# Performance work log

Hardware: AMD Instinct MI355X
Metric: run time of the kernel (lower is better)

Reference implementation:

```python
import jax, jax.numpy as jnp
import numpy as np

N, F, H, E, R = 100000, 256, 64, 800000, 7
EPS = 1e-5

def _layernorm(x, g, b):
    mu = jnp.mean(x, axis=-1, keepdims=True)
    var = jnp.mean((x - mu) ** 2, axis=-1, keepdims=True)
    return (x - mu) * jax.lax.rsqrt(var + EPS) * g + b

def setup_inputs() -> dict:
    key = jax.random.key(0)
    ks = jax.random.split(key, 16)
    block_features = jax.random.normal(ks[0], (N, F), dtype=jnp.float32)
    src = jax.random.randint(ks[1], (E,), 0, N).astype(jnp.float32)
    dst = jax.random.randint(ks[2], (E,), 0, N).astype(jnp.float32)
    rel = jax.random.randint(ks[3], (E,), 0, R).astype(jnp.float32)
    w = jax.random.uniform(ks[4], (E,), dtype=jnp.float32)
    typed_edges = jnp.stack([src, dst, rel, w], axis=1)  # [E,4]
    def lin(k, fan_in, fan_out):
        s = 1.0 / np.sqrt(fan_in)
        k1, k2 = jax.random.split(k)
        return (jax.random.uniform(k1, (fan_in, fan_out), jnp.float32, -s, s),
                jax.random.uniform(k2, (fan_out,), jnp.float32, -s, s))
    W1, b1 = lin(ks[5], F, H)
    W2, b2 = lin(ks[6], H, H)
    rel_emb = jax.random.normal(ks[7], (R, H), dtype=jnp.float32)
    Wm1, bm1 = lin(ks[8], 3 * H + 1, H)
    Wm2, bm2 = lin(ks[9], H, H)
    Wg1, bg1 = lin(ks[10], 2 * H, H)
    Wg2, bg2 = lin(ks[11], H, H)
    return dict(block_features=block_features, typed_edges=typed_edges,
                W1=W1, b1=b1, g1=jnp.ones(H), be1=jnp.zeros(H), W2=W2, b2=b2,
                rel_emb=rel_emb, Wm1=Wm1, bm1=bm1, Wm2=Wm2, bm2=bm2,
                gn=jnp.ones(H), bn=jnp.zeros(H), Wg1=Wg1, bg1=bg1, Wg2=Wg2, bg2=bg2)

def reference(block_features, typed_edges, W1, b1, g1, be1, W2, b2, rel_emb,
              Wm1, bm1, Wm2, bm2, gn, bn, Wg1, bg1, Wg2, bg2):
    # node_proj: Linear -> LN -> ReLU -> Linear -> ReLU
    h = jax.nn.relu(_layernorm(block_features @ W1 + b1, g1, be1))
    h = jax.nn.relu(h @ W2 + b2)  # [N,H]
    src = typed_edges[:, 0].astype(jnp.int32)
    dst = typed_edges[:, 1].astype(jnp.int32)
    rel = typed_edges[:, 2].astype(jnp.int32)
    w = typed_edges[:, 3:4]  # [E,1]
    m_in = jnp.concatenate([h[src], h[dst], rel_emb[rel], w], axis=-1)  # [E,3H+1]
    msg = jax.nn.relu(m_in @ Wm1 + bm1) @ Wm2 + bm2  # [E,H]
    agg = jax.ops.segment_sum(msg, dst, num_segments=h.shape[0])  # [N,H]
    nodes = _layernorm(h + agg, gn, bn)
    g = jnp.concatenate([nodes.mean(axis=0), nodes.max(axis=0)], axis=-1)  # [2H]
    return jax.nn.relu(g @ Wg1 + bg1) @ Wg2 + bg2  # [H]
```

## Files before the change

### kernel.cpp

```cpp
#include <hip/hip_runtime.h>

typedef unsigned short u16;
typedef unsigned int   u32;
typedef __attribute__((ext_vector_type(8))) short bf16x8;
typedef __attribute__((ext_vector_type(4))) float f32x4;

#define EPS 1e-5f
#define MFMA(a,b,c) __builtin_amdgcn_mfma_f32_16x16x32_bf16(a,b,c,0,0,0)

constexpr int OB_b1=0, OB_g1=64, OB_be1=128, OB_b2=192, OB_bm1=256, OB_w192=320,
              OB_bm2=384, OB_gn=448, OB_bn=512, OB_bg1=576, OB_bg2=640,
              OB_Wg1=704, OB_Wg2=8896, WB_TOT=12992;
constexpr int FR_Wm1=0;
constexpr int FR_Wm2=12288;
constexpr int FR_rel=16384;
constexpr int FR_W1 =16960;
constexpr int FR_W2 =33344;
constexpr int FR_TOT=37440;

__device__ __forceinline__ float bf2f(u32 u) { return __uint_as_float(u << 16); }
__device__ __forceinline__ u16 f2bf(float f) {
  u32 b = __float_as_uint(f);
  return (u16)((b + 0x7fffu + ((b >> 16) & 1u)) >> 16);
}
__device__ __forceinline__ u32 fkey(float f) {
  u32 b = __float_as_uint(f);
  return (b & 0x80000000u) ? ~b : (b | 0x80000000u);
}

__device__ __forceinline__ void gld_lds16(const void* g, void* l) {
  __builtin_amdgcn_global_load_lds(
      (const __attribute__((address_space(1))) void*)g,
      (__attribute__((address_space(3))) void*)l, 16, 0, 0);
}

__launch_bounds__(256)
__global__ void k_prep(const float* __restrict__ W1, const float* __restrict__ b1,
                       const float* __restrict__ g1, const float* __restrict__ be1,
                       const float* __restrict__ W2, const float* __restrict__ b2,
                       const float* __restrict__ rel_emb,
                       const float* __restrict__ Wm1, const float* __restrict__ bm1,
                       const float* __restrict__ Wm2, const float* __restrict__ bm2,
                       const float* __restrict__ gn, const float* __restrict__ bn,
                       const float* __restrict__ Wg1, const float* __restrict__ bg1,
                       const float* __restrict__ Wg2, const float* __restrict__ bg2,
                       float* __restrict__ wbuf, u16* __restrict__ frags,
                       const float* __restrict__ te, int* __restrict__ cnt,
                       float* __restrict__ gsum, u32* __restrict__ gmax, int E, int N) {
  int tid = blockIdx.x * 256 + threadIdx.x;
  int nth = gridDim.x * 256;
  for (int i = tid; i < 64; i += nth) {
    wbuf[OB_b1 + i] = b1[i];   wbuf[OB_g1 + i] = g1[i];
    wbuf[OB_be1 + i] = be1[i]; wbuf[OB_b2 + i] = b2[i];
    wbuf[OB_bm1 + i] = bm1[i]; wbuf[OB_w192 + i] = Wm1[192 * 64 + i];
    wbuf[OB_bm2 + i] = bm2[i]; wbuf[OB_gn + i] = gn[i];
    wbuf[OB_bn + i] = bn[i];   wbuf[OB_bg1 + i] = bg1[i];
    wbuf[OB_bg2 + i] = bg2[i];
    gsum[i] = 0.f; gmax[i] = 0u;
  }
  for (int i = tid; i < 8192; i += nth) wbuf[OB_Wg1 + i] = Wg1[i];
  for (int i = tid; i < 4096; i += nth) wbuf[OB_Wg2 + i] = Wg2[i];
  for (int idx = tid; idx < 16384; idx += nth) {
    int f = idx >> 9, L = (idx >> 3) & 63, j = idx & 7;
    int k = (f >> 2) * 32 + ((L >> 4) << 3) + j, n = ((f & 3) << 4) + (L & 15);
    frags[FR_W1 + idx] = f2bf(W1[k * 64 + n]);
  }
  for (int idx = tid; idx < 4096; idx += nth) {
    int f = idx >> 9, L = (idx >> 3) & 63, j = idx & 7;
    int k = (f >> 2) * 32 + ((L >> 4) << 3) + j, n = ((f & 3) << 4) + (L & 15);
    frags[FR_W2 + idx] = f2bf(W2[k * 64 + n]);
  }
  for (int idx = tid; idx < 12288; idx += nth) {
    int f = idx >> 9, L = (idx >> 3) & 63, j = idx & 7;
    int k = (f >> 2) * 32 + ((L >> 4) << 3) + j, n = ((f & 3) << 4) + (L & 15);
    frags[FR_Wm1 + idx] = f2bf(Wm1[k * 64 + n]);
  }
  for (int idx = tid; idx < 4096; idx += nth) {
    int f = idx >> 9, L = (idx >> 3) & 63, j = idx & 7;
    int k = (f >> 2) * 32 + ((L >> 4) << 3) + j, n = ((f & 3) << 4) + (L & 15);
    frags[FR_Wm2 + idx] = f2bf(Wm2[k * 64 + n]);
  }
  for (int idx = tid; idx < 576; idx += nth) {
    int r = idx / 80, c = idx % 80;
    frags[FR_rel + idx] = (r < 7 && c < 64) ? f2bf(rel_emb[r * 64 + c]) : (u16)0;
  }
  for (int e = tid; e < E; e += nth) {
    float4 v = *(const float4*)(te + (size_t)e * 4);
    int d = min(max((int)v.y, 0), N - 1);
    atomicAdd(&cnt[d], 1);
  }
}

#define SCH 512
__launch_bounds__(256)
__global__ void k_scan1(const int* __restrict__ cnt, int* __restrict__ bsum, int N) {
  __shared__ int sd[256];
  int b = blockIdx.x, t = threadIdx.x, base = b * SCH;
  int i0 = base + 2 * t, i1 = i0 + 1;
  int a = 0;
  if (i0 < N) a += cnt[i0];
  if (i1 < N) a += cnt[i1];
  sd[t] = a; __syncthreads();
  for (int s = 128; s > 0; s >>= 1) { if (t < s) sd[t] += sd[t + s]; __syncthreads(); }
  if (t == 0) bsum[b] = sd[0];
}

__launch_bounds__(256)
__global__ void k_scan2(const int* __restrict__ bsum, int* __restrict__ bofs,
                        int* __restrict__ ofs, int NBLK, int N) {
  __shared__ int sd[256];
  int t = threadIdx.x;
  int K = (NBLK + 255) / 256;
  int loc = 0;
  for (int k = 0; k < K; k++) { int i = t * K + k; if (i < NBLK) loc += bsum[i]; }
  sd[t] = loc; __syncthreads();
  for (int s = 1; s < 256; s <<= 1) {
    int o = 0; if (t >= s) o = sd[t - s];
    __syncthreads(); sd[t] += o; __syncthreads();
  }
  int excl = sd[t] - loc;
  int run = excl;
  for (int k = 0; k < K; k++) {
    int i = t * K + k;
    if (i < NBLK) { bofs[i] = run; run += bsum[i]; }
  }
  if (t == 255) ofs[N] = sd[255];
}

__launch_bounds__(256)
__global__ void k_scan3(const int* __restrict__ bofs, int* __restrict__ ofs,
                        int* __restrict__ cur, int N) {
  __shared__ int sd[256];
  int b = blockIdx.x, t = threadIdx.x, base = b * SCH;
  int i0 = base + 2 * t, i1 = i0 + 1;
  int a0 = (i0 < N) ? cur[i0] : 0, a1 = (i1 < N) ? cur[i1] : 0;
  int pair = a0 + a1;
  sd[t] = pair; __syncthreads();
  for (int s = 1; s < 256; s <<= 1) {
    int o = 0; if (t >= s) o = sd[t - s];
    __syncthreads(); sd[t] += o; __syncthreads();
  }
  int excl = sd[t] - pair + bofs[b];
  if (i0 < N) { ofs[i0] = excl;      cur[i0] = excl; }
  if (i1 < N) { ofs[i1] = excl + a0; cur[i1] = excl + a0; }
}

__launch_bounds__(256)
__global__ void k_place(const float* __restrict__ te, int* __restrict__ cur,
                        uint4* __restrict__ sorted, int E, int N) {
  int i = blockIdx.x * 256 + threadIdx.x, st = gridDim.x * 256;
  for (int e = i; e < E; e += st) {
    float4 v = *(const float4*)(te + (size_t)e * 4);
    int s = min(max((int)v.x, 0), N - 1);
    int d = min(max((int)v.y, 0), N - 1);
    int r = min(max((int)v.z, 0), 6);
    int pos = atomicAdd(&cur[d], 1);
    uint4 rec; rec.x = (u32)s; rec.y = (u32)d; rec.z = (u32)r; rec.w = __float_as_uint(v.w);
    sorted[pos] = rec;
  }
}

__launch_bounds__(256, 4)
__global__ void k_h(const float* __restrict__ X, const float* __restrict__ wbuf,
                    const u16* __restrict__ frags, u16* __restrict__ hb,
                    float* __restrict__ agg, int N) {
  __shared__ __align__(16) float xb[2][16 * 256];
  __shared__ __align__(16) u16 st[16 * 72];
  __shared__ float sred[2][16][4];

  int lane = threadIdx.x & 63, wave = threadIdx.x >> 6;
  int m = lane & 15, quad = lane >> 4;
  int col = wave * 16 + m;

  bf16x8 bw1[8], bw2[2];
  #pragma unroll
  for (int ks = 0; ks < 8; ks++)
    bw1[ks] = *(const bf16x8*)(frags + FR_W1 + ((ks * 4 + wave) * 64 + lane) * 8);
  #pragma unroll
  for (int ks = 0; ks < 2; ks++)
    bw2[ks] = *(const bf16x8*)(frags + FR_W2 + ((ks * 4 + wave) * 64 + lane) * 8);

  float b1v = wbuf[OB_b1 + col], g1v = wbuf[OB_g1 + col];
  float be1v = wbuf[OB_be1 + col], b2v = wbuf[OB_b2 + col];

  int ntiles = (N + 15) / 16;
  int xorm = (m & 7) << 4;

  auto stage = [&](int t, int buf) {
    int n0s = t * 16;
    #pragma unroll
    for (int i = 0; i < 4; i++) {
      int r = wave * 4 + i;
      int nr = min(n0s + r, N - 1);
      const char* src = (const char*)(X + (size_t)nr * 256);
      int soff = (lane * 16) ^ ((r & 7) << 4);
      gld_lds16(src + soff, (char*)&xb[buf][0] + r * 1024);
    }
  };

  int cur = 0;
  if (blockIdx.x < ntiles) stage(blockIdx.x, 0);

  for (int t = blockIdx.x; t < ntiles; t += gridDim.x) {
    __syncthreads();
    if (t + (int)gridDim.x < ntiles) stage(t + gridDim.x, cur ^ 1);

    int n0 = t * 16;
    const char* xp = (const char*)&xb[cur][0];

    f32x4 acc = {};
    #pragma unroll
    for (int ks = 0; ks < 8; ks++) {
      int base = m * 1024 + ks * 128 + quad * 32;
      float4 u0 = *(const float4*)(xp + (base ^ xorm));
      float4 u1 = *(const float4*)(xp + ((base + 16) ^ xorm));
      bf16x8 a;
      a[0] = (short)f2bf(u0.x); a[1] = (short)f2bf(u0.y);
      a[2] = (short)f2bf(u0.z); a[3] = (short)f2bf(u0.w);
      a[4] = (short)f2bf(u1.x); a[5] = (short)f2bf(u1.y);
      a[6] = (short)f2bf(u1.z); a[7] = (short)f2bf(u1.w);
      acc = MFMA(a, bw1[ks], acc);
    }

    float vv[4];
    #pragma unroll
    for (int r = 0; r < 4; r++) vv[r] = acc[r] + b1v;
    #pragma unroll
    for (int r = 0; r < 4; r++) {
      float s = vv[r], q = vv[r] * vv[r];
      #pragma unroll
      for (int mk = 8; mk >= 1; mk >>= 1) {
        s += __shfl_xor(s, mk, 64);
        q += __shfl_xor(q, mk, 64);
      }
      if (m == 0) { sred[0][quad * 4 + r][wave] = s; sred[1][quad * 4 + r][wave] = q; }
    }
    __syncthreads();
    #pragma unroll
    for (int r = 0; r < 4; r++) {
      int row = quad * 4 + r;
      float4 S = *(const float4*)&sred[0][row][0];
      float4 Q = *(const float4*)&sred[1][row][0];
      float mu = (S.x + S.y + S.z + S.w) * (1.f / 64.f);
      float vq = (Q.x + Q.y + Q.z + Q.w) * (1.f / 64.f) - mu * mu;
      float rs = rsqrtf(fmaxf(vq, 0.f) + EPS);
      float h1 = fmaxf(fmaf((vv[r] - mu) * rs, g1v, be1v), 0.f);
      st[row * 72 + col] = f2bf(h1);
    }
    __syncthreads();

    f32x4 acc2 = {};
    #pragma unroll
    for (int ks = 0; ks < 2; ks++) {
      bf16x8 a2 = *(const bf16x8*)(st + m * 72 + ks * 32 + quad * 8);
      acc2 = MFMA(a2, bw2[ks], acc2);
    }
    #pragma unroll
    for (int r = 0; r < 4; r++) {
      int row = n0 + quad * 4 + r;
      if (row < N) {
        float hv = fmaxf(acc2[r] + b2v, 0.f);
        hb[(size_t)row * 64 + col] = f2bf(hv);
        agg[(size_t)row * 64 + col] = hv;
      }
    }
    cur ^= 1;
  }
}

__launch_bounds__(512, 4)
__global__ void k_edge(const uint4* __restrict__ sorted, const u16* __restrict__ hb,
                       const float* __restrict__ wbuf, const u16* __restrict__ frags,
                       float* __restrict__ agg, int E, int N) {
  __shared__ __align__(16) u16 sWm1[24 * 512];
  __shared__ __align__(16) u16 sWm2[8 * 512];
  __shared__ __align__(16) u16 srel[576];
  __shared__ __align__(16) float st32[8][16 * 68];
  __shared__ int sdst[8][16];

  {
    const uint4* s1 = (const uint4*)(frags + FR_Wm1);
    uint4* d1 = (uint4*)sWm1;
    for (int i = threadIdx.x; i < 1536; i += 512) d1[i] = s1[i];
    const uint4* s2 = (const uint4*)(frags + FR_Wm2);
    uint4* d2 = (uint4*)sWm2;
    for (int i = threadIdx.x; i < 512; i += 512) d2[i] = s2[i];
    const uint4* s3 = (const uint4*)(frags + FR_rel);
    uint4* d3 = (uint4*)srel;
    for (int i = threadIdx.x; i < 72; i += 512) d3[i] = s3[i];
  }
  __syncthreads();

  int lane = threadIdx.x & 63, wave = threadIdx.x >> 6;
  int m = lane & 15, quad = lane >> 4, koff = quad * 8, col0 = m;
  float* st = st32[wave];
  int* dstS = sdst[wave];

  float bm1v[4], w192v[4], bm2v[4];
  #pragma unroll
  for (int nt = 0; nt < 4; nt++) {
    int c = nt * 16 + col0;
    bm1v[nt] = wbuf[OB_bm1 + c];
    w192v[nt] = wbuf[OB_w192 + c];
    bm2v[nt] = wbuf[OB_bm2 + c];
  }

  int ntiles = (E + 15) >> 4;
  int gw = blockIdx.x * 8 + wave, nw = gridDim.x * 8;
  int per = (ntiles + nw - 1) / nw;
  int tile = gw * per, tend = min(tile + per, ntiles);

  int cd = -1; float cv = 0.f;

  for (; tile < tend; tile++) {
    int e0 = tile * 16;
    int src = 0, dstv = 0, rel = 0; float w = 0.f;
    if (lane < 16) {
      int e = e0 + lane;
      uint4 rc = sorted[min(e, E - 1)];
      src = (int)rc.x; dstv = (int)rc.y; rel = (int)rc.z; w = __uint_as_float(rc.w);
      dstS[lane] = (e < E) ? dstv : -1;
    }
    int sm = __shfl(src, m, 64), dm = __shfl(dstv, m, 64), rm = __shfl(rel, m, 64);

    const u16* hs = hb + (size_t)sm * 64;
    const u16* hd = hb + (size_t)dm * 64;
    bf16x8 af[6];
    af[0] = *(const bf16x8*)(hs + koff);
    af[1] = *(const bf16x8*)(hs + 32 + koff);
    af[2] = *(const bf16x8*)(hd + koff);
    af[3] = *(const bf16x8*)(hd + 32 + koff);
    af[4] = *(const bf16x8*)(srel + rm * 80 + koff);
    af[5] = *(const bf16x8*)(srel + rm * 80 + 32 + koff);

    f32x4 acc[4] = {};
    #pragma unroll
    for (int ks = 0; ks < 6; ks++)
      #pragma unroll
      for (int nt = 0; nt < 4; nt++) {
        bf16x8 b = *(const bf16x8*)(sWm1 + (ks * 4 + nt) * 512 + lane * 8);
        acc[nt] = MFMA(af[ks], b, acc[nt]);
      }

    float wrow[4];
    #pragma unroll
    for (int r = 0; r < 4; r++) wrow[r] = __shfl(w, quad * 4 + r, 64);
    #pragma unroll
    for (int nt = 0; nt < 4; nt++)
      #pragma unroll
      for (int r = 0; r < 4; r++) {
        float v = fmaf(wrow[r], w192v[nt], acc[nt][r] + bm1v[nt]);
        st[(quad * 4 + r) * 68 + nt * 16 + col0] = fmaxf(v, 0.f);
      }
    __builtin_amdgcn_wave_barrier();

    f32x4 acc2[4] = {};
    #pragma unroll
    for (int ks = 0; ks < 2; ks++) {
      float4 p0 = *(const float4*)(st + m * 68 + ks * 32 + koff);
      float4 p1 = *(const float4*)(st + m * 68 + ks * 32 + koff + 4);
      bf16x8 a2;
      a2[0] = (short)f2bf(p0.x); a2[1] = (short)f2bf(p0.y);
      a2[2] = (short)f2bf(p0.z); a2[3] = (short)f2bf(p0.w);
      a2[4] = (short)f2bf(p1.x); a2[5] = (short)f2bf(p1.y);
      a2[6] = (short)f2bf(p1.z); a2[7] = (short)f2bf(p1.w);
      #pragma unroll
      for (int nt = 0; nt < 4; nt++) {
        bf16x8 b = *(const bf16x8*)(sWm2 + (ks * 4 + nt) * 512 + lane * 8);
        acc2[nt] = MFMA(a2, b, acc2[nt]);
      }
    }
    __builtin_amdgcn_wave_barrier();

    #pragma unroll
    for (int nt = 0; nt < 4; nt++)
      #pragma unroll
      for (int r = 0; r < 4; r++)
        st[(quad * 4 + r) * 68 + nt * 16 + col0] = acc2[nt][r] + bm2v[nt];
    __builtin_amdgcn_wave_barrier();

    #pragma unroll
    for (int r = 0; r < 16; r++) {
      int d = dstS[r];
      float v = st[r * 68 + lane];
      if (d != cd) {
        if (cd >= 0) atomicAdd(agg + (size_t)cd * 64 + lane, cv);
        cd = d; cv = 0.f;
      }
      if (d >= 0) cv += v;
    }
    __builtin_amdgcn_wave_barrier();
  }
  if (cd >= 0) atomicAdd(agg + (size_t)cd * 64 + lane, cv);
}

__launch_bounds__(256)
__global__ void k_nodes(const float* __restrict__ agg, const float* __restrict__ wbuf,
                        float* __restrict__ gsum, u32* __restrict__ gmax, int N) {
  int lane = threadIdx.x & 63, wave = threadIdx.x >> 6;
  int r4 = lane >> 4, c4 = (lane & 15) * 4;
  float4 gnv = *(const float4*)(wbuf + OB_gn + c4);
  float4 bnv = *(const float4*)(wbuf + OB_bn + c4);
  int wid = blockIdx.x * 4 + wave, nw = gridDim.x * 4;
  float sj[4] = {0.f, 0.f, 0.f, 0.f};
  float mj[4] = {-3.0e38f, -3.0e38f, -3.0e38f, -3.0e38f};
  for (int base = wid * 4; base < N; base += nw * 4) {
    int row = base + r4;
    bool ok = row < N;
    float4 av = ok ? *(const float4*)(agg + (size_t)row * 64 + c4)
                   : make_float4(0.f, 0.f, 0.f, 0.f);
    float s = av.x + av.y + av.z + av.w;
    #pragma unroll
    for (int mk = 8; mk >= 1; mk >>= 1) s += __shfl_xor(s, mk, 64);
    float mu = s * (1.f / 64.f);
    float d0 = av.x - mu, d1 = av.y - mu, d2 = av.z - mu, d3 = av.w - mu;
    float q = d0 * d0 + d1 * d1 + d2 * d2 + d3 * d3;
    #pragma unroll
    for (int mk = 8; mk >= 1; mk >>= 1) q += __shfl_xor(q, mk, 64);
    float rs = rsqrtf(q * (1.f / 64.f) + EPS);
    if (ok) {
      float t0 = fmaf(d0 * rs, gnv.x, bnv.x);
      float t1 = fmaf(d1 * rs, gnv.y, bnv.y);
      float t2 = fmaf(d2 * rs, gnv.z, bnv.z);
      float t3 = fmaf(d3 * rs, gnv.w, bnv.w);
      sj[0] += t0; mj[0] = fmaxf(mj[0], t0);
      sj[1] += t1; mj[1] = fmaxf(mj[1], t1);
      sj[2] += t2; mj[2] = fmaxf(mj[2], t2);
      sj[3] += t3; mj[3] = fmaxf(mj[3], t3);
    }
  }
  #pragma unroll
  for (int j = 0; j < 4; j++) {
    sj[j] += __shfl_xor(sj[j], 16, 64);
    sj[j] += __shfl_xor(sj[j], 32, 64);
    mj[j] = fmaxf(mj[j], __shfl_xor(mj[j], 16, 64));
    mj[j] = fmaxf(mj[j], __shfl_xor(mj[j], 32, 64));
  }
  __shared__ float bs[4][64], bm[4][64];
  if (lane < 16) {
    #pragma unroll
    for (int j = 0; j < 4; j++) { bs[wave][c4 + j] = sj[j]; bm[wave][c4 + j] = mj[j]; }
  }
  __syncthreads();
  if (threadIdx.x < 64) {
    int c = threadIdx.x;
    float ts = bs[0][c] + bs[1][c] + bs[2][c] + bs[3][c];
    float tm = fmaxf(fmaxf(bm[0][c], bm[1][c]), fmaxf(bm[2][c], bm[3][c]));
    atomicAdd(gsum + c, ts);
    atomicMax(gmax + c, fkey(tm));
  }
}

__launch_bounds__(128)
__global__ void k_final(const float* __restrict__ wbuf, const float* __restrict__ gsum,
                        const u32* __restrict__ gmax, float* __restrict__ out, int N) {
  __shared__ float g[128];
  __shared__ float y1[64];
  int t = threadIdx.x;
  if (t < 64) {
    g[t] = gsum[t] / (float)N;
  } else {
    u32 k = gmax[t - 64];
    u32 b = (k & 0x80000000u) ? (k & 0x7fffffffu) : ~k;
    g[t] = __uint_as_float(b);
  }
  __syncthreads();
  if (t < 64) {
    float a = wbuf[OB_bg1 + t];
    for (int i = 0; i < 128; i++) a = fmaf(g[i], wbuf[OB_Wg1 + i * 64 + t], a);
    y1[t] = fmaxf(a, 0.f);
  }
  __syncthreads();
  if (t < 64) {
    float a = wbuf[OB_bg2 + t];
    for (int k = 0; k < 64; k++) a = fmaf(y1[k], wbuf[OB_Wg2 + k * 64 + t], a);
    out[t] = a;
  }
}

extern "C" void kernel_launch(void* const* d_in, const int* in_sizes, int n_in,
                              void* d_out, int out_size, void* d_ws, size_t ws_size,
                              hipStream_t stream) {
  const int N = in_sizes[0] / 256;
  const int E = in_sizes[1] / 4;
  const int NBLK = (N + SCH - 1) / SCH;

  char* ws = (char*)d_ws;
  size_t p = 0;
  auto rup = [](size_t x) { return (x + 255) & ~(size_t)255; };
  uint4* sorted = (uint4*)(ws + p); p += rup((size_t)E * 16);
  float* agg    = (float*)(ws + p); p += rup((size_t)N * 64 * 4);
  u16*   hb     = (u16*)(ws + p);   p += rup((size_t)N * 128);
  int*   ofs    = (int*)(ws + p);   p += rup((size_t)(N + 1) * 4);
  int*   cur    = (int*)(ws + p);   p += rup((size_t)N * 4);
  int*   bsum   = (int*)(ws + p);   p += rup((size_t)(NBLK + 1) * 4);
  int*   bofs   = (int*)(ws + p);   p += rup((size_t)(NBLK + 1) * 4);
  float* gsum   = (float*)(ws + p); p += 256;
  u32*   gmax   = (u32*)(ws + p);   p += 256;
  float* wbuf   = (float*)(ws + p); p += rup((size_t)WB_TOT * 4);
  u16*   frags  = (u16*)(ws + p);   p += rup((size_t)FR_TOT * 2);

  const float* X  = (const float*)d_in[0];
  const float* te = (const float*)d_in[1];

  hipMemsetAsync(cur, 0, (size_t)N * 4, stream);
  hipLaunchKernelGGL(k_prep, dim3(1024), dim3(256), 0, stream,
                     (const float*)d_in[2], (const float*)d_in[3], (const float*)d_in[4],
                     (const float*)d_in[5], (const float*)d_in[6], (const float*)d_in[7],
                     (const float*)d_in[8], (const float*)d_in[9], (const float*)d_in[10],
                     (const float*)d_in[11], (const float*)d_in[12], (const float*)d_in[13],
                     (const float*)d_in[14], (const float*)d_in[15], (const float*)d_in[16],
                     (const float*)d_in[17], (const float*)d_in[18], wbuf, frags,
                     te, cur, gsum, gmax, E, N);

  hipLaunchKernelGGL(k_scan1, dim3(NBLK), dim3(256), 0, stream, cur, bsum, N);
  hipLaunchKernelGGL(k_scan2, dim3(1), dim3(256), 0, stream, bsum, bofs, ofs, NBLK, N);
  hipLaunchKernelGGL(k_scan3, dim3(NBLK), dim3(256), 0, stream, bofs, ofs, cur, N);
  hipLaunchKernelGGL(k_place, dim3(1024), dim3(256), 0, stream, te, cur, sorted, E, N);

  hipLaunchKernelGGL(k_h, dim3(1024), dim3(256), 0, stream, X, wbuf, frags, hb, agg, N);
  hipLaunchKernelGGL(k_edge, dim3(512), dim3(512), 0, stream, sorted, hb, wbuf, frags, agg, E, N);
  hipLaunchKernelGGL(k_nodes, dim3(2048), dim3(256), 0, stream, agg, wbuf, gsum, gmax, N);
  hipLaunchKernelGGL(k_final, dim3(1), dim3(128), 0, stream, wbuf, gsum, gmax, (float*)d_out, N);
}
```

Baseline: 400.6 us.

## Merge scan kernels, prefetch edge tiles, fuse final MLP into nodes kernel

Replaces the three-pass prefix scan with one single-block 1024-thread scan and folds the final MLP into k_nodes using a last-block ticket, removing several kernel launches. k_edge now prefetches the next tile's edge records and gathered features while the current tile's MFMAs run. It keeps the hidden activations as bf16 in LDS instead of fp32, and moves the scatter through register shuffles instead of an LDS round trip. Occupancy and grid size for k_edge go up (launch bounds 5, grid 768). The single-block scan serializes about 100 elements per thread, and the prefetch adds register pressure.

New measurement: 594.2 us. +48.3%, slower.

```diff
diff --git a/kernel.cpp b/kernel.cpp
--- a/kernel.cpp
+++ b/kernel.cpp
@@ -46,9 +46,11 @@
                        const float* __restrict__ Wg2, const float* __restrict__ bg2,
                        float* __restrict__ wbuf, u16* __restrict__ frags,
                        const float* __restrict__ te, int* __restrict__ cnt,
-                       float* __restrict__ gsum, u32* __restrict__ gmax, int E, int N) {
+                       float* __restrict__ gsum, u32* __restrict__ gmax,
+                       int* __restrict__ ticket, int E, int N) {
   int tid = blockIdx.x * 256 + threadIdx.x;
   int nth = gridDim.x * 256;
+  if (tid == 0) *ticket = 0;
   for (int i = tid; i < 64; i += nth) {
     wbuf[OB_b1 + i] = b1[i];   wbuf[OB_g1 + i] = g1[i];
     wbuf[OB_be1 + i] = be1[i]; wbuf[OB_b2 + i] = b2[i];
@@ -91,58 +93,27 @@
   }
 }
 
-#define SCH 512
-__launch_bounds__(256)
-__global__ void k_scan1(const int* __restrict__ cnt, int* __restrict__ bsum, int N) {
-  __shared__ int sd[256];
-  int b = blockIdx.x, t = threadIdx.x, base = b * SCH;
-  int i0 = base + 2 * t, i1 = i0 + 1;
-  int a = 0;
-  if (i0 < N) a += cnt[i0];
-  if (i1 < N) a += cnt[i1];
-  sd[t] = a; __syncthreads();
-  for (int s = 128; s > 0; s >>= 1) { if (t < s) sd[t] += sd[t + s]; __syncthreads(); }
-  if (t == 0) bsum[b] = sd[0];
-}
-
-__launch_bounds__(256)
-__global__ void k_scan2(const int* __restrict__ bsum, int* __restrict__ bofs,
-                        int* __restrict__ ofs, int NBLK, int N) {
-  __shared__ int sd[256];
+__launch_bounds__(1024)
+__global__ void k_scan(int* __restrict__ cur, int N) {
+  __shared__ int sd[1024];
   int t = threadIdx.x;
-  int K = (NBLK + 255) / 256;
+  int K = (N + 1023) / 1024;
+  int beg = t * K, end = min(beg + K, N);
   int loc = 0;
-  for (int k = 0; k < K; k++) { int i = t * K + k; if (i < NBLK) loc += bsum[i]; }
+  for (int i = beg; i < end; i++) loc += cur[i];
   sd[t] = loc; __syncthreads();
-  for (int s = 1; s < 256; s <<= 1) {
-    int o = 0; if (t >= s) o = sd[t - s];
-    __syncthreads(); sd[t] += o; __syncthreads();
-  }
-  int excl = sd[t] - loc;
-  int run = excl;
-  for (int k = 0; k < K; k++) {
-    int i = t * K + k;
-    if (i < NBLK) { bofs[i] = run; run += bsum[i]; }
-  }
-  if (t == 255) ofs[N] = sd[255];
-}
-
-__launch_bounds__(256)
-__global__ void k_scan3(const int* __restrict__ bofs, int* __restrict__ ofs,
-                        int* __restrict__ cur, int N) {
-  __shared__ int sd[256];
-  int b = blockIdx.x, t = threadIdx.x, base = b * SCH;
-  int i0 = base + 2 * t, i1 = i0 + 1;
-  int a0 = (i0 < N) ? cur[i0] : 0, a1 = (i1 < N) ? cur[i1] : 0;
-  int pair = a0 + a1;
-  sd[t] = pair; __syncthreads();
-  for (int s = 1; s < 256; s <<= 1) {
-    int o = 0; if (t >= s) o = sd[t - s];
-    __syncthreads(); sd[t] += o; __syncthreads();
-  }
-  int excl = sd[t] - pair + bofs[b];
-  if (i0 < N) { ofs[i0] = excl;      cur[i0] = excl; }
-  if (i1 < N) { ofs[i1] = excl + a0; cur[i1] = excl + a0; }
+  for (int s = 1; s < 1024; s <<= 1) {
+    int o = (t >= s) ? sd[t - s] : 0;
+    __syncthreads();
+    sd[t] += o;
+    __syncthreads();
+  }
+  int run = sd[t] - loc;
+  for (int i = beg; i < end; i++) {
+    int c = cur[i];
+    cur[i] = run;
+    run += c;
+  }
 }
 
 __launch_bounds__(256)
@@ -268,15 +239,14 @@
   }
 }
 
-__launch_bounds__(512, 4)
+__launch_bounds__(512, 5)
 __global__ void k_edge(const uint4* __restrict__ sorted, const u16* __restrict__ hb,
                        const float* __restrict__ wbuf, const u16* __restrict__ frags,
                        float* __restrict__ agg, int E, int N) {
   __shared__ __align__(16) u16 sWm1[24 * 512];
   __shared__ __align__(16) u16 sWm2[8 * 512];
   __shared__ __align__(16) u16 srel[576];
-  __shared__ __align__(16) float st32[8][16 * 68];
-  __shared__ int sdst[8][16];
+  __shared__ __align__(16) u16 stt[8][16 * 72];
 
   {
     const uint4* s1 = (const uint4*)(frags + FR_Wm1);
@@ -293,8 +263,8 @@
 
   int lane = threadIdx.x & 63, wave = threadIdx.x >> 6;
   int m = lane & 15, quad = lane >> 4, koff = quad * 8, col0 = m;
-  float* st = st32[wave];
-  int* dstS = sdst[wave];
+  int nthi = lane >> 4;
+  u16* stw = stt[wave];
 
   float bm1v[4], w192v[4], bm2v[4];
   #pragma unroll
@@ -306,32 +276,44 @@
   }
 
   int ntiles = (E + 15) >> 4;
-  int gw = blockIdx.x * 8 + wave, nw = gridDim.x * 8;
-  int per = (ntiles + nw - 1) / nw;
+  int gw = blockIdx.x * 8 + wave, nwv = gridDim.x * 8;
+  int per = (ntiles + nwv - 1) / nwv;
   int tile = gw * per, tend = min(tile + per, ntiles);
 
   int cd = -1; float cv = 0.f;
-
-  for (; tile < tend; tile++) {
-    int e0 = tile * 16;
-    int src = 0, dstv = 0, rel = 0; float w = 0.f;
+  int dstv = -1; float wv = 0.f;
+  bf16x8 af[6];
+
+  if (tile < tend) {
+    int srcv = 0, relv = 0;
     if (lane < 16) {
-      int e = e0 + lane;
+      int e = tile * 16 + lane;
       uint4 rc = sorted[min(e, E - 1)];
-      src = (int)rc.x; dstv = (int)rc.y; rel = (int)rc.z; w = __uint_as_float(rc.w);
-      dstS[lane] = (e < E) ? dstv : -1;
-    }
-    int sm = __shfl(src, m, 64), dm = __shfl(dstv, m, 64), rm = __shfl(rel, m, 64);
-
+      srcv = (int)rc.x; dstv = (e < E) ? (int)rc.y : -1;
+      relv = (int)rc.z; wv = __uint_as_float(rc.w);
+    }
+    int sm = __shfl(srcv, m, 64), dmv = __shfl(dstv, m, 64), rm = __shfl(relv, m, 64);
+    int dmg = dmv < 0 ? 0 : dmv;
     const u16* hs = hb + (size_t)sm * 64;
-    const u16* hd = hb + (size_t)dm * 64;
-    bf16x8 af[6];
+    const u16* hd = hb + (size_t)dmg * 64;
     af[0] = *(const bf16x8*)(hs + koff);
     af[1] = *(const bf16x8*)(hs + 32 + koff);
     af[2] = *(const bf16x8*)(hd + koff);
     af[3] = *(const bf16x8*)(hd + 32 + koff);
     af[4] = *(const bf16x8*)(srel + rm * 80 + koff);
     af[5] = *(const bf16x8*)(srel + rm * 80 + 32 + koff);
+  }
+
+  for (; tile < tend; tile++) {
+    bool hasnext = (tile + 1) < tend;
+
+    int srcn = 0, dstn = -1, reln = 0; float wn = 0.f;
+    if (hasnext && lane < 16) {
+      int e = (tile + 1) * 16 + lane;
+      uint4 rc = sorted[min(e, E - 1)];
+      srcn = (int)rc.x; dstn = (e < E) ? (int)rc.y : -1;
+      reln = (int)rc.z; wn = __uint_as_float(rc.w);
+    }
 
     f32x4 acc[4] = {};
     #pragma unroll
@@ -342,28 +324,35 @@
         acc[nt] = MFMA(af[ks], b, acc[nt]);
       }
 
+    if (hasnext) {
+      int sm = __shfl(srcn, m, 64), dmv = __shfl(dstn, m, 64), rm = __shfl(reln, m, 64);
+      int dmg = dmv < 0 ? 0 : dmv;
+      const u16* hs = hb + (size_t)sm * 64;
+      const u16* hd = hb + (size_t)dmg * 64;
+      af[0] = *(const bf16x8*)(hs + koff);
+      af[1] = *(const bf16x8*)(hs + 32 + koff);
+      af[2] = *(const bf16x8*)(hd + koff);
+      af[3] = *(const bf16x8*)(hd + 32 + koff);
+      af[4] = *(const bf16x8*)(srel + rm * 80 + koff);
+      af[5] = *(const bf16x8*)(srel + rm * 80 + 32 + koff);
+    }
+
     float wrow[4];
     #pragma unroll
-    for (int r = 0; r < 4; r++) wrow[r] = __shfl(w, quad * 4 + r, 64);
+    for (int r = 0; r < 4; r++) wrow[r] = __shfl(wv, quad * 4 + r, 64);
     #pragma unroll
     for (int nt = 0; nt < 4; nt++)
       #pragma unroll
       for (int r = 0; r < 4; r++) {
         float v = fmaf(wrow[r], w192v[nt], acc[nt][r] + bm1v[nt]);
-        st[(quad * 4 + r) * 68 + nt * 16 + col0] = fmaxf(v, 0.f);
+        stw[(quad * 4 + r) * 72 + nt * 16 + col0] = f2bf(fmaxf(v, 0.f));
       }
     __builtin_amdgcn_wave_barrier();
 
     f32x4 acc2[4] = {};
     #pragma unroll
     for (int ks = 0; ks < 2; ks++) {
-      float4 p0 = *(const float4*)(st + m * 68 + ks * 32 + koff);
-      float4 p1 = *(const float4*)(st + m * 68 + ks * 32 + koff + 4);
-      bf16x8 a2;
-      a2[0] = (short)f2bf(p0.x); a2[1] = (short)f2bf(p0.y);
-      a2[2] = (short)f2bf(p0.z); a2[3] = (short)f2bf(p0.w);
-      a2[4] = (short)f2bf(p1.x); a2[5] = (short)f2bf(p1.y);
-      a2[6] = (short)f2bf(p1.z); a2[7] = (short)f2bf(p1.w);
+      bf16x8 a2 = *(const bf16x8*)(stw + m * 72 + ks * 32 + koff);
       #pragma unroll
       for (int nt = 0; nt < 4; nt++) {
         bf16x8 b = *(const bf16x8*)(sWm2 + (ks * 4 + nt) * 512 + lane * 8);
@@ -373,30 +362,30 @@
     __builtin_amdgcn_wave_barrier();
 
     #pragma unroll
-    for (int nt = 0; nt < 4; nt++)
-      #pragma unroll
-      for (int r = 0; r < 4; r++)
-        st[(quad * 4 + r) * 68 + nt * 16 + col0] = acc2[nt][r] + bm2v[nt];
-    __builtin_amdgcn_wave_barrier();
-
-    #pragma unroll
     for (int r = 0; r < 16; r++) {
-      int d = dstS[r];
-      float v = st[r * 68 + lane];
+      int d = __shfl(dstv, r, 64);
+      int sl = ((r >> 2) << 4) + m;
+      float c0 = __shfl(acc2[0][r & 3] + bm2v[0], sl, 64);
+      float c1 = __shfl(acc2[1][r & 3] + bm2v[1], sl, 64);
+      float c2 = __shfl(acc2[2][r & 3] + bm2v[2], sl, 64);
+      float c3 = __shfl(acc2[3][r & 3] + bm2v[3], sl, 64);
+      float v = nthi == 0 ? c0 : nthi == 1 ? c1 : nthi == 2 ? c2 : c3;
       if (d != cd) {
         if (cd >= 0) atomicAdd(agg + (size_t)cd * 64 + lane, cv);
         cd = d; cv = 0.f;
       }
       if (d >= 0) cv += v;
     }
-    __builtin_amdgcn_wave_barrier();
+
+    dstv = dstn; wv = wn;
   }
   if (cd >= 0) atomicAdd(agg + (size_t)cd * 64 + lane, cv);
 }
 
 __launch_bounds__(256)
 __global__ void k_nodes(const float* __restrict__ agg, const float* __restrict__ wbuf,
-                        float* __restrict__ gsum, u32* __restrict__ gmax, int N) {
+                        float* __restrict__ gsum, u32* __restrict__ gmax,
+                        int* __restrict__ ticket, float* __restrict__ out, int N) {
   int lane = threadIdx.x & 63, wave = threadIdx.x >> 6;
   int r4 = lane >> 4, c4 = (lane & 15) * 4;
   float4 gnv = *(const float4*)(wbuf + OB_gn + c4);
@@ -449,32 +438,38 @@
     atomicAdd(gsum + c, ts);
     atomicMax(gmax + c, fkey(tm));
   }
-}
-
-__launch_bounds__(128)
-__global__ void k_final(const float* __restrict__ wbuf, const float* __restrict__ gsum,
-                        const u32* __restrict__ gmax, float* __restrict__ out, int N) {
-  __shared__ float g[128];
-  __shared__ float y1[64];
-  int t = threadIdx.x;
-  if (t < 64) {
-    g[t] = gsum[t] / (float)N;
-  } else {
-    u32 k = gmax[t - 64];
-    u32 b = (k & 0x80000000u) ? (k & 0x7fffffffu) : ~k;
-    g[t] = __uint_as_float(b);
-  }
   __syncthreads();
-  if (t < 64) {
-    float a = wbuf[OB_bg1 + t];
-    for (int i = 0; i < 128; i++) a = fmaf(g[i], wbuf[OB_Wg1 + i * 64 + t], a);
-    y1[t] = fmaxf(a, 0.f);
+
+  __shared__ int slast;
+  if (threadIdx.x == 0) {
+    __threadfence();
+    slast = atomicAdd(ticket, 1);
   }
   __syncthreads();
-  if (t < 64) {
-    float a = wbuf[OB_bg2 + t];
-    for (int k = 0; k < 64; k++) a = fmaf(y1[k], wbuf[OB_Wg2 + k * 64 + t], a);
-    out[t] = a;
+  if (slast == (int)gridDim.x - 1) {
+    __threadfence();
+    __shared__ float g[128];
+    __shared__ float y1[64];
+    int t = threadIdx.x;
+    if (t < 64) {
+      g[t] = atomicAdd(gsum + t, 0.f) / (float)N;
+    } else if (t < 128) {
+      u32 k = atomicOr(gmax + (t - 64), 0u);
+      u32 b = (k & 0x80000000u) ? (k & 0x7fffffffu) : ~k;
+      g[t] = __uint_as_float(b);
+    }
+    __syncthreads();
+    if (t < 64) {
+      float a = wbuf[OB_bg1 + t];
+      for (int i = 0; i < 128; i++) a = fmaf(g[i], wbuf[OB_Wg1 + i * 64 + t], a);
+      y1[t] = fmaxf(a, 0.f);
+    }
+    __syncthreads();
+    if (t < 64) {
+      float a = wbuf[OB_bg2 + t];
+      for (int k = 0; k < 64; k++) a = fmaf(y1[k], wbuf[OB_Wg2 + k * 64 + t], a);
+      out[t] = a;
+    }
   }
 }
 
@@ -483,7 +478,6 @@
                               hipStream_t stream) {
   const int N = in_sizes[0] / 256;
   const int E = in_sizes[1] / 4;
-  const int NBLK = (N + SCH - 1) / SCH;
 
   char* ws = (char*)d_ws;
   size_t p = 0;
@@ -491,12 +485,10 @@
   uint4* sorted = (uint4*)(ws + p); p += rup((size_t)E * 16);
   float* agg    = (float*)(ws + p); p += rup((size_t)N * 64 * 4);
   u16*   hb     = (u16*)(ws + p);   p += rup((size_t)N * 128);
-  int*   ofs    = (int*)(ws + p);   p += rup((size_t)(N + 1) * 4);
   int*   cur    = (int*)(ws + p);   p += rup((size_t)N * 4);
-  int*   bsum   = (int*)(ws + p);   p += rup((size_t)(NBLK + 1) * 4);
-  int*   bofs   = (int*)(ws + p);   p += rup((size_t)(NBLK + 1) * 4);
   float* gsum   = (float*)(ws + p); p += 256;
   u32*   gmax   = (u32*)(ws + p);   p += 256;
+  int*   ticket = (int*)(ws + p);   p += 256;
   float* wbuf   = (float*)(ws + p); p += rup((size_t)WB_TOT * 4);
   u16*   frags  = (u16*)(ws + p);   p += rup((size_t)FR_TOT * 2);
 
@@ -511,15 +503,13 @@
                      (const float*)d_in[11], (const float*)d_in[12], (const float*)d_in[13],
                      (const float*)d_in[14], (const float*)d_in[15], (const float*)d_in[16],
                      (const float*)d_in[17], (const float*)d_in[18], wbuf, frags,
-                     te, cur, gsum, gmax, E, N);
-
-  hipLaunchKernelGGL(k_scan1, dim3(NBLK), dim3(256), 0, stream, cur, bsum, N);
-  hipLaunchKernelGGL(k_scan2, dim3(1), dim3(256), 0, stream, bsum, bofs, ofs, NBLK, N);
-  hipLaunchKernelGGL(k_scan3, dim3(NBLK), dim3(256), 0, stream, bofs, ofs, cur, N);
+                     te, cur, gsum, gmax, ticket, E, N);
+
+  hipLaunchKernelGGL(k_scan, dim3(1), dim3(1024), 0, stream, cur, N);
   hipLaunchKernelGGL(k_place, dim3(1024), dim3(256), 0, stream, te, cur, sorted, E, N);
 
   hipLaunchKernelGGL(k_h, dim3(1024), dim3(256), 0, stream, X, wbuf, frags, hb, agg, N);
-  hipLaunchKernelGGL(k_edge, dim3(512), dim3(512), 0, stream, sorted, hb, wbuf, frags, agg, E, N);
-  hipLaunchKernelGGL(k_nodes, dim3(2048), dim3(256), 0, stream, agg, wbuf, gsum, gmax, N);
-  hipLaunchKernelGGL(k_final, dim3(1), dim3(128), 0, stream, wbuf, gsum, gmax, (float*)d_out, N);
-}
+  hipLaunchKernelGGL(k_edge, dim3(768), dim3(512), 0, stream, sorted, hb, wbuf, frags, agg, E, N);
+  hipLaunchKernelGGL(k_nodes, dim3(2048), dim3(256), 0, stream, agg, wbuf, gsum, gmax,
+                     ticket, (float*)d_out, N);
+}
```
